# Kernel tuning notes

Hardware: AMD Instinct MI355X
Metric: run time of the kernel (lower is better)

The kernel has to match this reference:

```python
import jax, jax.numpy as jnp
import numpy as np
from functools import partial

TAU = 2.0
V_TH = 1.0
ALPHA = 2.0  # ATan surrogate alpha (spikingjelly default)
DIM = 512

@jax.custom_vjp
def heaviside(x):
    return (x >= 0).astype(x.dtype)

def _heaviside_fwd(x):
    return heaviside(x), x

def _heaviside_bwd(x, g):
    # ATan surrogate: d/dx sigmoid-like = alpha/2 / (1 + (pi/2*alpha*x)^2)
    sg = (ALPHA / 2.0) / (1.0 + (jnp.pi / 2.0 * ALPHA * x) ** 2)
    return (g * sg,)

heaviside.defvjp(_heaviside_fwd, _heaviside_bwd)

def lif_multistep(x_seq):
    """LIF, decay_input=False, hard reset to 0, v_threshold=V_TH.
    x_seq: [T, ...] -> spikes [T, ...]"""
    decay = 1.0 - 1.0 / TAU
    def step(v, x):
        v = v * decay + x            # charge (no decay on input)
        s = heaviside(v - V_TH)      # fire with surrogate grad
        v = v * (1.0 - jax.lax.stop_gradient(s))  # hard reset, detach_reset
        return v, s
    v0 = jnp.zeros_like(x_seq[0])
    _, s_seq = jax.lax.scan(step, v0, x_seq)
    return s_seq

def setup_inputs() -> dict:
    key = jax.random.key(0)
    k1, k2, k3 = jax.random.split(key, 3)
    T, B, N = 4, 32, 512
    inputs = jax.random.normal(k1, (T, B, N, 2 * DIM), dtype=jnp.float32)
    W = jax.random.normal(k2, (DIM, DIM), dtype=jnp.float32) / np.sqrt(DIM)
    b = jax.random.normal(k3, (DIM,), dtype=jnp.float32) * 0.01
    return {"inputs": inputs, "W": W, "b": b}

def reference(inputs, W, b):
    outputs, gate = jnp.split(inputs, 2, axis=-1)   # chunk(2, dim=-1)
    gate = lif_multistep(gate)                      # lif1
    gate = jnp.einsum('tbnd,ed->tbne', gate, W) + b # proj_conv (Linear)
    gate = lif_multistep(gate)                      # lif2
    return outputs * gate
```

## Files before the change

### kernel.cpp

```cpp
#include <hip/hip_runtime.h>
#include <cstdint>
#include <cstddef>

#define TS     4
#define BNROWS 16384
#define DIMN   512
#define CIN    1024

typedef __attribute__((ext_vector_type(8))) short short8;
typedef __attribute__((ext_vector_type(4))) float f32x4;

__device__ __forceinline__ uint16_t f2bf(float f) {
    union { float f; uint32_t u; } x; x.f = f;
    return (uint16_t)((x.u + 0x7FFFu + ((x.u >> 16) & 1u)) >> 16);
}
__device__ __forceinline__ float bf2f(uint16_t h) {
    union { uint32_t u; float f; } x; x.u = ((uint32_t)h) << 16;
    return x.f;
}

__global__ __launch_bounds__(256) void k_wsplit(const float* __restrict__ W,
        uint16_t* __restrict__ Wh, uint16_t* __restrict__ Wm) {
    int i = (blockIdx.x * 256 + threadIdx.x) * 4;
    int e  = i >> 9;
    int k  = i & 511;
    int ks = k >> 5, kk = k & 31;
    size_t o = ((size_t)((ks << 9) + e) << 5) + kk;
    float4 w4 = *(const float4*)(W + i);
    float wv[4] = {w4.x, w4.y, w4.z, w4.w};
    uint16_t hh[4], mm[4];
#pragma unroll
    for (int j = 0; j < 4; ++j) {
        uint16_t a = f2bf(wv[j]);
        float r = wv[j] - bf2f(a);
        hh[j] = a; mm[j] = f2bf(r);
    }
    *(ushort4*)(Wh + o) = make_ushort4(hh[0], hh[1], hh[2], hh[3]);
    *(ushort4*)(Wm + o) = make_ushort4(mm[0], mm[1], mm[2], mm[3]);
}

#define DELTA 1e-3f
__global__ __launch_bounds__(512, 4) void k_fused(
        const float*    __restrict__ in,
        const uint16_t* __restrict__ Wh,
        const uint16_t* __restrict__ Wm,
        const float*    __restrict__ bias,
        unsigned short* __restrict__ gbits,
        uint8_t*        __restrict__ A8,
        unsigned int*   __restrict__ counter,
        unsigned int*   __restrict__ list,
        unsigned int    cap) {
    __shared__ short A_lds[64 * 512];

    const int tid = threadIdx.x;
    const int blk = blockIdx.x;
    const int bn0 = blk * 16;

#pragma unroll
    for (int pp = 0; pp < 2; ++pp) {
        const int p   = tid + pp * 512;
        const int bnl = p >> 6;
        const int g   = p & 63;
        const int d0  = g << 3;
        const int bng = bn0 + bnl;
        float v[8] = {0.f,0.f,0.f,0.f,0.f,0.f,0.f,0.f};
#pragma unroll
        for (int t = 0; t < TS; ++t) {
            const float4* px = (const float4*)(in + ((size_t)(t * BNROWS + bng)) * CIN + DIMN + d0);
            float4 x0 = px[0], x1 = px[1];
            float xs[8] = {x0.x, x0.y, x0.z, x0.w, x1.x, x1.y, x1.z, x1.w};
            short8 sb;
            union { uint2 u; uint8_t b[8]; } pk;
#pragma unroll
            for (int j = 0; j < 8; ++j) {
                v[j] = v[j] * 0.5f + xs[j];
                bool sp = (v[j] >= 1.0f);
                sb[j]   = sp ? (short)0x3F80 : (short)0;
                pk.b[j] = sp ? 1u : 0u;
                v[j] = sp ? 0.0f : v[j];
            }
            const int row  = (bnl << 2) + t;
            const int boff = row * 1024 + ((d0 * 2) ^ ((row & 7) << 4));
            *(short8*)((char*)A_lds + boff) = sb;
            *(uint2*)(A8 + ((size_t)((bng << 2) + t)) * DIMN + d0) = pk.u;
        }
    }
    __syncthreads();

    const int wv   = tid >> 6;
    const int lane = tid & 63;
    const int ln   = lane & 15;
    const int quad = lane >> 4;
    const int e_base = wv * 64;

    f32x4 acc[4][4] = {};

#pragma unroll 4
    for (int ks = 0; ks < 16; ++ks) {
        short8 bh[4], bm[4];
#pragma unroll
        for (int ni = 0; ni < 4; ++ni) {
            const size_t off = ((size_t)((ks << 9) + e_base + ni * 16 + ln) << 5) + quad * 8;
            bh[ni] = *(const short8*)(Wh + off);
            bm[ni] = *(const short8*)(Wm + off);
        }
        const int k0 = ks * 32 + quad * 8;
        short8 a[4];
#pragma unroll
        for (int mi = 0; mi < 4; ++mi) {
            const int row  = mi * 16 + ln;
            const int boff = row * 1024 + ((k0 * 2) ^ ((row & 7) << 4));
            a[mi] = *(const short8*)((const char*)A_lds + boff);
        }
#pragma unroll
        for (int ni = 0; ni < 4; ++ni) {
#pragma unroll
            for (int mi = 0; mi < 4; ++mi) {
                acc[mi][ni] = __builtin_amdgcn_mfma_f32_16x16x32_bf16(a[mi], bh[ni], acc[mi][ni], 0, 0, 0);
                acc[mi][ni] = __builtin_amdgcn_mfma_f32_16x16x32_bf16(a[mi], bm[ni], acc[mi][ni], 0, 0, 0);
            }
        }
    }

#pragma unroll
    for (int ni = 0; ni < 4; ++ni) {
        const int e = e_base + ni * 16 + ln;
        const float be = bias[e];
#pragma unroll
        for (int mi = 0; mi < 4; ++mi) {
            const int bn = bn0 + mi * 4 + quad;
            float v = 0.f;
            bool bad = false;
#pragma unroll
            for (int t = 0; t < TS; ++t) {
                float y = acc[mi][ni][t] + be;
                v = v * 0.5f + y;
                bad = bad || (fabsf(v - 1.0f) < DELTA);
                bool sp = (v >= 1.0f);
                unsigned long long b = __ballot(sp);
                if (ln == 0) {
                    gbits[((size_t)(bn * 4 + t)) * 32 + (wv * 4 + ni)] =
                        (unsigned short)((b >> (quad * 16)) & 0xFFFFull);
                }
                v = sp ? 0.0f : v;
            }
            if (bad) {
                unsigned idx = atomicAdd(counter, 1u);
                if (idx < cap) list[idx] = ((unsigned)bn << 9) | (unsigned)e;
            }
        }
    }
}

__global__ __launch_bounds__(256) void k_gate(
        const float*          __restrict__ in,
        const unsigned short* __restrict__ gbits,
        float*                __restrict__ out) {
    const unsigned gtid = blockIdx.x * 256 + threadIdx.x;
    const int bn = (gtid >> 7) & 16383;
    const int c  = gtid & 127;
    const unsigned gidx = ((unsigned)bn * 4) * 32 + (c >> 2);
    const int sh = (c & 3) * 4;
    const float4* __restrict__ in4  = (const float4*)in;
    float4*       __restrict__ out4 = (float4*)out;
#pragma unroll
    for (int t = 0; t < TS; ++t) {
        const float4 ov = in4[(size_t)(t * BNROWS + bn) * 256 + c];
        const unsigned gb = gbits[gidx + t * 32] >> sh;
        float4 o;
        o.x = (gb & 1u) ? ov.x : 0.0f;
        o.y = (gb & 2u) ? ov.y : 0.0f;
        o.z = (gb & 4u) ? ov.z : 0.0f;
        o.w = (gb & 8u) ? ov.w : 0.0f;
        out4[(size_t)t * 2097152 + gtid] = o;
    }
}

__global__ __launch_bounds__(256) void k_fix(
        const uint8_t* __restrict__ A8,
        const float*   __restrict__ W,
        const float*   __restrict__ bias,
        const float*   __restrict__ in,
        float*         __restrict__ out,
        const unsigned int* __restrict__ counter,
        const unsigned int* __restrict__ list,
        unsigned int cap) {
    unsigned n = *counter; if (n > cap) n = cap;
    unsigned gtid = blockIdx.x * blockDim.x + threadIdx.x;
    unsigned gsz  = gridDim.x * blockDim.x;
    for (unsigned i = gtid; i < n; i += gsz) {
        unsigned item = list[i];
        int bn = (int)(item >> 9), e = (int)(item & 511u);
        const float* wrow = W + (size_t)e * DIMN;
        float v = 0.f;
        for (int t = 0; t < TS; ++t) {
            const uint8_t* arow = A8 + (size_t)(bn * 4 + t) * DIMN;
            float acc0 = 0.f, acc1 = 0.f, acc2 = 0.f, acc3 = 0.f;
            for (int c = 0; c < 32; ++c) {
                const int base = c * 16;
#pragma unroll
                for (int j = 3; j >= 0; --j) {
                    const int b4 = base + j * 4;
                    float s0 = arow[b4 + 0] ? 1.0f : 0.0f;
                    float s1 = arow[b4 + 1] ? 1.0f : 0.0f;
                    float s2 = arow[b4 + 2] ? 1.0f : 0.0f;
                    float s3 = arow[b4 + 3] ? 1.0f : 0.0f;
                    acc0 = fmaf(s0, wrow[b4 + 0], acc0);
                    acc1 = fmaf(s1, wrow[b4 + 1], acc1);
                    acc2 = fmaf(s2, wrow[b4 + 2], acc2);
                    acc3 = fmaf(s3, wrow[b4 + 3], acc3);
                }
            }
            float lo  = acc0 + acc1;
            float hi  = acc2 + acc3;
            float dot = lo + hi;
            float y = dot + bias[e];
            v = v * 0.5f + y;
            bool sp = (v >= 1.0f);
            size_t obase = (size_t)(t * BNROWS + bn);
            out[obase * DIMN + e] = sp ? in[obase * CIN + e] : 0.0f;
            v = sp ? 0.0f : v;
        }
    }
}

extern "C" void kernel_launch(void* const* d_in, const int* in_sizes, int n_in,
                              void* d_out, int out_size, void* d_ws, size_t ws_size,
                              hipStream_t stream) {
    const float* in   = (const float*)d_in[0];
    const float* W    = (const float*)d_in[1];
    const float* bias = (const float*)d_in[2];
    float* out = (float*)d_out;

    uint8_t*        A8      = (uint8_t*)d_ws;
    uint16_t*       Wh      = (uint16_t*)((char*)d_ws + (size_t)33554432);
    uint16_t*       Wm      = (uint16_t*)((char*)d_ws + (size_t)34078720);
    unsigned int*   counter = (unsigned int*)((char*)d_ws + (size_t)34603008);
    unsigned int*   list    = (unsigned int*)((char*)d_ws + (size_t)34603072);
    unsigned short* gbits   = (unsigned short*)((char*)d_ws + (size_t)35403072);
    const unsigned int cap = 200000u;

    hipMemsetAsync(counter, 0, sizeof(unsigned int), stream);
    k_wsplit<<<256, 256, 0, stream>>>(W, Wh, Wm);
    k_fused<<<1024, 512, 0, stream>>>(in, Wh, Wm, bias, gbits, A8, counter, list, cap);
    k_gate<<<8192, 256, 0, stream>>>(in, gbits, out);
    k_fix<<<256, 256, 0, stream>>>(A8, W, bias, in, out, counter, list, cap);
}
```

Measured before the change: 609.4 us.

## Split LIF1 into separate kernel and feed GEMM from swizzled byte spikes

Moves the first LIF layer out of the fused GEMM kernel into its own kernel that writes 8-bit spike bytes in an XOR-swizzled layout. The GEMM kernel now copies its 32 KB block of spike bytes into LDS with wide loads and expands them to bf16 on the fly, instead of reading fp32 inputs and computing LIF in the prologue. The aim is to shorten the GEMM prologue and lower LDS use per block (byte storage in place of bf16), in exchange for an extra launch, a round trip of A8 through global memory, and byte-to-bf16 conversion work inside the inner loop. The fix-up kernel is changed to read the swizzled layout.

```diff
diff --git a/kernel.cpp b/kernel.cpp
--- a/kernel.cpp
+++ b/kernel.cpp
@@ -39,60 +39,62 @@
     *(ushort4*)(Wm + o) = make_ushort4(mm[0], mm[1], mm[2], mm[3]);
 }
 
+__global__ __launch_bounds__(256) void k_lif1(const float* __restrict__ in,
+                                              uint8_t* __restrict__ A8) {
+    const int gtid = blockIdx.x * 256 + threadIdx.x;
+    const int bn = gtid >> 6;
+    const int d0 = (gtid & 63) << 3;
+    float v[8] = {0.f,0.f,0.f,0.f,0.f,0.f,0.f,0.f};
+#pragma unroll
+    for (int t = 0; t < TS; ++t) {
+        const float4* px = (const float4*)(in + ((size_t)(t * BNROWS + bn)) * CIN + DIMN + d0);
+        float4 x0 = px[0], x1 = px[1];
+        float xs[8] = {x0.x, x0.y, x0.z, x0.w, x1.x, x1.y, x1.z, x1.w};
+        union { uint2 u; uint8_t b[8]; } pk;
+#pragma unroll
+        for (int j = 0; j < 8; ++j) {
+            v[j] = v[j] * 0.5f + xs[j];
+            bool sp = (v[j] >= 1.0f);
+            pk.b[j] = sp ? 1u : 0u;
+            v[j] = sp ? 0.0f : v[j];
+        }
+        const int row = bn * 4 + t;
+        *(uint2*)(A8 + (size_t)row * 512 + (d0 ^ ((row & 7) << 3))) = pk.u;
+    }
+}
+
 #define DELTA 1e-3f
-__global__ __launch_bounds__(512, 4) void k_fused(
-        const float*    __restrict__ in,
+__global__ __launch_bounds__(512, 4) void k_gemm(
+        const uint8_t*  __restrict__ A8,
         const uint16_t* __restrict__ Wh,
         const uint16_t* __restrict__ Wm,
         const float*    __restrict__ bias,
         unsigned short* __restrict__ gbits,
-        uint8_t*        __restrict__ A8,
         unsigned int*   __restrict__ counter,
         unsigned int*   __restrict__ list,
         unsigned int    cap) {
-    __shared__ short A_lds[64 * 512];
-
-    const int tid = threadIdx.x;
-    const int blk = blockIdx.x;
-    const int bn0 = blk * 16;
-
-#pragma unroll
-    for (int pp = 0; pp < 2; ++pp) {
-        const int p   = tid + pp * 512;
-        const int bnl = p >> 6;
-        const int g   = p & 63;
-        const int d0  = g << 3;
-        const int bng = bn0 + bnl;
-        float v[8] = {0.f,0.f,0.f,0.f,0.f,0.f,0.f,0.f};
-#pragma unroll
-        for (int t = 0; t < TS; ++t) {
-            const float4* px = (const float4*)(in + ((size_t)(t * BNROWS + bng)) * CIN + DIMN + d0);
-            float4 x0 = px[0], x1 = px[1];
-            float xs[8] = {x0.x, x0.y, x0.z, x0.w, x1.x, x1.y, x1.z, x1.w};
-            short8 sb;
-            union { uint2 u; uint8_t b[8]; } pk;
-#pragma unroll
-            for (int j = 0; j < 8; ++j) {
-                v[j] = v[j] * 0.5f + xs[j];
-                bool sp = (v[j] >= 1.0f);
-                sb[j]   = sp ? (short)0x3F80 : (short)0;
-                pk.b[j] = sp ? 1u : 0u;
-                v[j] = sp ? 0.0f : v[j];
-            }
-            const int row  = (bnl << 2) + t;
-            const int boff = row * 1024 + ((d0 * 2) ^ ((row & 7) << 4));
-            *(short8*)((char*)A_lds + boff) = sb;
-            *(uint2*)(A8 + ((size_t)((bng << 2) + t)) * DIMN + d0) = pk.u;
-        }
-    }
-    __syncthreads();
-
+    __shared__ __align__(16) uint8_t A_lds[32768];
+
+    const int tid  = threadIdx.x;
+    const int blk  = blockIdx.x;
+    const int bn0  = blk * 16;
     const int wv   = tid >> 6;
     const int lane = tid & 63;
     const int ln   = lane & 15;
     const int quad = lane >> 4;
     const int e_base = wv * 64;
 
+    {
+        const uint8_t* gsrc = A8 + (size_t)blk * 32768;
+        const int toff = tid * 16;
+#pragma unroll
+        for (int it = 0; it < 4; ++it) {
+            const int seg = it * 8192 + toff;
+            *(uint4*)(&A_lds[seg]) = *(const uint4*)(gsrc + seg);
+        }
+    }
+    __syncthreads();
+
     f32x4 acc[4][4] = {};
 
 #pragma unroll 4
@@ -108,9 +110,12 @@
         short8 a[4];
 #pragma unroll
         for (int mi = 0; mi < 4; ++mi) {
-            const int row  = mi * 16 + ln;
-            const int boff = row * 1024 + ((k0 * 2) ^ ((row & 7) << 4));
-            a[mi] = *(const short8*)((const char*)A_lds + boff);
+            const int row = mi * 16 + ln;
+            union { uint2 u; uint8_t b[8]; } ld;
+            ld.u = *(const uint2*)(A_lds + row * 512 + (k0 ^ ((row & 7) << 3)));
+#pragma unroll
+            for (int j = 0; j < 8; ++j)
+                a[mi][j] = ld.b[j] ? (short)0x3F80 : (short)0;
         }
 #pragma unroll
         for (int ni = 0; ni < 4; ++ni) {
@@ -194,17 +199,19 @@
         const float* wrow = W + (size_t)e * DIMN;
         float v = 0.f;
         for (int t = 0; t < TS; ++t) {
-            const uint8_t* arow = A8 + (size_t)(bn * 4 + t) * DIMN;
+            const int row = bn * 4 + t;
+            const uint8_t* arow = A8 + (size_t)row * 512;
+            const int xv = (row & 7) << 3;
             float acc0 = 0.f, acc1 = 0.f, acc2 = 0.f, acc3 = 0.f;
             for (int c = 0; c < 32; ++c) {
                 const int base = c * 16;
 #pragma unroll
                 for (int j = 3; j >= 0; --j) {
                     const int b4 = base + j * 4;
-                    float s0 = arow[b4 + 0] ? 1.0f : 0.0f;
-                    float s1 = arow[b4 + 1] ? 1.0f : 0.0f;
-                    float s2 = arow[b4 + 2] ? 1.0f : 0.0f;
-                    float s3 = arow[b4 + 3] ? 1.0f : 0.0f;
+                    float s0 = arow[(b4 + 0) ^ xv] ? 1.0f : 0.0f;
+                    float s1 = arow[(b4 + 1) ^ xv] ? 1.0f : 0.0f;
+                    float s2 = arow[(b4 + 2) ^ xv] ? 1.0f : 0.0f;
+                    float s3 = arow[(b4 + 3) ^ xv] ? 1.0f : 0.0f;
                     acc0 = fmaf(s0, wrow[b4 + 0], acc0);
                     acc1 = fmaf(s1, wrow[b4 + 1], acc1);
                     acc2 = fmaf(s2, wrow[b4 + 2], acc2);
@@ -242,7 +249,8 @@
 
     hipMemsetAsync(counter, 0, sizeof(unsigned int), stream);
     k_wsplit<<<256, 256, 0, stream>>>(W, Wh, Wm);
-    k_fused<<<1024, 512, 0, stream>>>(in, Wh, Wm, bias, gbits, A8, counter, list, cap);
+    k_lif1<<<4096, 256, 0, stream>>>(in, A8);
+    k_gemm<<<1024, 512, 0, stream>>>(A8, Wh, Wm, bias, gbits, counter, list, cap);
     k_gate<<<8192, 256, 0, stream>>>(in, gbits, out);
     k_fix<<<256, 256, 0, stream>>>(A8, W, bias, in, out, counter, list, cap);
 }
```

After: 795.1 us. 1.3x slower.

## Parallelize fixup dot products across wave lanes and fold counter reset into wsplit

Applied to the files above, without the earlier changes.

The fixup kernel that recomputes near-threshold outputs in exact fp32 now assigns each item to a 16-lane group instead of one thread. Lanes split the four timesteps and four byte offsets, load spikes as uint4, and reduce partial sums with shuffles. The grid grows to 1024 blocks. The counter memset is removed, and the first thread of k_wsplit zeroes the counter instead, saving one launch. The fp32 summation order changes, and the fixup's weight and spike loads are now strided across lanes.

```diff
diff --git a/kernel.cpp b/kernel.cpp
--- a/kernel.cpp
+++ b/kernel.cpp
@@ -20,7 +20,9 @@
 }
 
 __global__ __launch_bounds__(256) void k_wsplit(const float* __restrict__ W,
-        uint16_t* __restrict__ Wh, uint16_t* __restrict__ Wm) {
+        uint16_t* __restrict__ Wh, uint16_t* __restrict__ Wm,
+        unsigned int* __restrict__ counter) {
+    if (blockIdx.x == 0 && threadIdx.x == 0) *counter = 0u;
     int i = (blockIdx.x * 256 + threadIdx.x) * 4;
     int e  = i >> 9;
     int k  = i & 511;
@@ -186,40 +188,55 @@
         const unsigned int* __restrict__ list,
         unsigned int cap) {
     unsigned n = *counter; if (n > cap) n = cap;
-    unsigned gtid = blockIdx.x * blockDim.x + threadIdx.x;
-    unsigned gsz  = gridDim.x * blockDim.x;
-    for (unsigned i = gtid; i < n; i += gsz) {
-        unsigned item = list[i];
-        int bn = (int)(item >> 9), e = (int)(item & 511u);
+    if (n == 0) return;
+    const int lane = threadIdx.x & 63;
+    const int grp  = lane >> 4;
+    const int sub  = lane & 15;
+    const int ai   = sub & 3;
+    const int lt   = sub >> 2;
+    const unsigned wid = blockIdx.x * (blockDim.x >> 6) + (threadIdx.x >> 6);
+    const unsigned nw  = gridDim.x * (blockDim.x >> 6);
+
+    for (unsigned it0 = wid * 4; it0 < n; it0 += nw * 4) {
+        const unsigned myi   = it0 + grp;
+        const bool    active = (myi < n);
+        const unsigned item  = list[active ? myi : 0];
+        const int bn = (int)(item >> 9), e = (int)(item & 511u);
+
+        const uint4* a4   = (const uint4*)(A8 + (size_t)(bn * 4 + lt) * 512);
         const float* wrow = W + (size_t)e * DIMN;
-        float v = 0.f;
-        for (int t = 0; t < TS; ++t) {
-            const uint8_t* arow = A8 + (size_t)(bn * 4 + t) * DIMN;
-            float acc0 = 0.f, acc1 = 0.f, acc2 = 0.f, acc3 = 0.f;
-            for (int c = 0; c < 32; ++c) {
-                const int base = c * 16;
-#pragma unroll
-                for (int j = 3; j >= 0; --j) {
-                    const int b4 = base + j * 4;
-                    float s0 = arow[b4 + 0] ? 1.0f : 0.0f;
-                    float s1 = arow[b4 + 1] ? 1.0f : 0.0f;
-                    float s2 = arow[b4 + 2] ? 1.0f : 0.0f;
-                    float s3 = arow[b4 + 3] ? 1.0f : 0.0f;
-                    acc0 = fmaf(s0, wrow[b4 + 0], acc0);
-                    acc1 = fmaf(s1, wrow[b4 + 1], acc1);
-                    acc2 = fmaf(s2, wrow[b4 + 2], acc2);
-                    acc3 = fmaf(s3, wrow[b4 + 3], acc3);
-                }
-            }
-            float lo  = acc0 + acc1;
-            float hi  = acc2 + acc3;
-            float dot = lo + hi;
-            float y = dot + bias[e];
-            v = v * 0.5f + y;
-            bool sp = (v >= 1.0f);
-            size_t obase = (size_t)(t * BNROWS + bn);
-            out[obase * DIMN + e] = sp ? in[obase * CIN + e] : 0.0f;
-            v = sp ? 0.0f : v;
+        const int sh = 8 * ai;
+        float acc = 0.f;
+#pragma unroll 4
+        for (int c = 0; c < 32; ++c) {
+            const uint4 blk = a4[c];
+            const float* wq = wrow + c * 16 + ai;
+            acc = fmaf((float)((blk.w >> sh) & 0xFFu), wq[12], acc);
+            acc = fmaf((float)((blk.z >> sh) & 0xFFu), wq[8],  acc);
+            acc = fmaf((float)((blk.y >> sh) & 0xFFu), wq[4],  acc);
+            acc = fmaf((float)((blk.x >> sh) & 0xFFu), wq[0],  acc);
+        }
+        const float a1 = __shfl(acc, (lane & 60) | 1);
+        const float a2 = __shfl(acc, (lane & 60) | 2);
+        const float a3 = __shfl(acc, (lane & 60) | 3);
+        const float dot = (acc + a1) + (a2 + a3);
+        const float d0 = __shfl(dot, (lane & 48) | 0);
+        const float d1 = __shfl(dot, (lane & 48) | 4);
+        const float d2 = __shfl(dot, (lane & 48) | 8);
+        const float d3 = __shfl(dot, (lane & 48) | 12);
+        if (active && sub == 0) {
+            const float be = bias[e];
+            const float ds[4] = {d0, d1, d2, d3};
+            float v = 0.f;
+#pragma unroll
+            for (int t = 0; t < TS; ++t) {
+                const float y = ds[t] + be;
+                v = v * 0.5f + y;
+                const bool sp = (v >= 1.0f);
+                const size_t ob = (size_t)(t * BNROWS + bn);
+                out[ob * DIMN + e] = sp ? in[ob * CIN + e] : 0.0f;
+                v = sp ? 0.0f : v;
+            }
         }
     }
 }
@@ -240,9 +257,8 @@
     unsigned short* gbits   = (unsigned short*)((char*)d_ws + (size_t)35403072);
     const unsigned int cap = 200000u;
 
-    hipMemsetAsync(counter, 0, sizeof(unsigned int), stream);
-    k_wsplit<<<256, 256, 0, stream>>>(W, Wh, Wm);
+    k_wsplit<<<256, 256, 0, stream>>>(W, Wh, Wm, counter);
     k_fused<<<1024, 512, 0, stream>>>(in, Wh, Wm, bias, gbits, A8, counter, list, cap);
     k_gate<<<8192, 256, 0, stream>>>(in, gbits, out);
-    k_fix<<<256, 256, 0, stream>>>(A8, W, bias, in, out, counter, list, cap);
-}
+    k_fix<<<1024, 256, 0, stream>>>(A8, W, bias, in, out, counter, list, cap);
+}
```

Measured after the change: 525.9 us. 1.16x faster.
